# Optimization experiments

Measured on AMD Instinct MI355X. Metric: run time of the kernel, lower is better.

Reference implementation:

```python
import jax, jax.numpy as jnp
import numpy as np

E = 1024  # embed_dim
NH = 16   # num_heads
HH, WW = 128, 128


def setup_inputs() -> dict:
    key = jax.random.key(0)
    ks = jax.random.split(key, 9)
    s = 0.02
    x = jax.random.normal(ks[0], (1, HH, WW, E), dtype=jnp.float32)
    d = {"x": x}
    for i, name in enumerate(["q", "k", "v", "o"]):
        d[f"W{name}"] = jax.random.normal(ks[1 + 2 * i], (E, E), dtype=jnp.float32) * s
        d[f"b{name}"] = jax.random.normal(ks[2 + 2 * i], (E,), dtype=jnp.float32) * s
    return d


def reference(x, Wq, bq, Wk, bk, Wv, bv, Wo, bo):
    B, h, w, e = x.shape
    D = e // NH  # head dim
    # projections + ReLU feature map on q, k (torch Linear: x @ W.T + b)
    q = jnp.maximum(x @ Wq.T + bq, 0.0).reshape(B, h, w, NH, D)
    k = jnp.maximum(x @ Wk.T + bk, 0.0).reshape(B, h, w, NH, D)
    v = (x @ Wv.T + bv).reshape(B, h, w, NH, D)
    # width-axis linear retention: kv state per (row h, head n)
    kv_w = jnp.einsum('bhwnd,bhwne->bhnde', k, v)        # [B,h,NH,D,D]
    out = jnp.einsum('bhwnd,bhnde->bhwne', q, kv_w)      # [B,h,w,NH,D]
    # height-axis linear retention: kv state per (col w, head n)
    kv_h = jnp.einsum('bhwnd,bhwne->bwnde', k, v)        # [B,w,NH,D,D]
    out = jnp.einsum('bhwne,bwnef->bhwnf', out, kv_h)    # [B,h,w,NH,D]
    out = out.reshape(B, h, w, e) @ Wo.T + bo
    return out.reshape(B, h * w, e)
```

## Files before the change

### kernel.cpp

```cpp
#include <hip/hip_runtime.h>
#include <hip/hip_bf16.h>
#include <stdint.h>


typedef __attribute__((ext_vector_type(4))) float floatx4;
typedef __attribute__((ext_vector_type(8))) short shortx8;

static __device__ __forceinline__ unsigned short f2bf(float f) {
  unsigned int u = __float_as_uint(f);
  u += 0x7fffu + ((u >> 16) & 1u);
  return (unsigned short)(u >> 16);
}

static __device__ __forceinline__ void gload16(const void* g, void* l) {
  __builtin_amdgcn_global_load_lds(
      (const __attribute__((address_space(1))) void*)g,
      (__attribute__((address_space(3))) void*)l, 16, 0, 0);
}

__global__ __launch_bounds__(256) void cvt_all(
    const float* __restrict__ x, const float* __restrict__ Wq,
    const float* __restrict__ Wk, const float* __restrict__ Wv,
    const float* __restrict__ Wo, unsigned short* __restrict__ xb,
    unsigned short* __restrict__ wqkvb, unsigned short* __restrict__ wob) {
  const int b = blockIdx.x;
  const float* src;
  unsigned short* dst;
  int off;
  if (b < 16384) {
    src = x; dst = xb; off = b;
  } else if (b < 17408) {
    src = Wq; dst = wqkvb; off = b - 16384;
  } else if (b < 18432) {
    src = Wk; dst = wqkvb + 1048576; off = b - 17408;
  } else if (b < 19456) {
    src = Wv; dst = wqkvb + 2097152; off = b - 18432;
  } else {
    src = Wo; dst = wob; off = b - 19456;
  }
  const int i = (off * 256 + threadIdx.x) * 4;
  float4 f = *(const float4*)(src + i);
  ushort4 o;
  o.x = f2bf(f.x); o.y = f2bf(f.y); o.z = f2bf(f.z); o.w = f2bf(f.w);
  *(ushort4*)(dst + i) = o;
}

#define BARRIER()                           \
  do {                                      \
    asm volatile("" ::: "memory");          \
    __builtin_amdgcn_s_barrier();           \
    asm volatile("" ::: "memory");          \
  } while (0)
#define LGKM0 asm volatile("s_waitcnt lgkmcnt(0)" ::: "memory")
#define VMCNT(N) asm volatile("s_waitcnt vmcnt(" #N ")" ::: "memory")

template <int MODE>
__global__ __launch_bounds__(512, 2) void gemm256(
    const unsigned short* __restrict__ A,
    const unsigned short* __restrict__ BT,
    const float* __restrict__ b0, const float* __restrict__ b1,
    const float* __restrict__ b2,
    unsigned short* __restrict__ Oq, unsigned short* __restrict__ Ok,
    unsigned short* __restrict__ Ov, float* __restrict__ Of) {
  __shared__ __align__(16) unsigned short smem[65536];
  const int t = threadIdx.x;
  const int lane = t & 63, wid = t >> 6;
  const int wm = wid >> 2, wn = wid & 3;
  const int mrow = lane & 15, quad = lane >> 4;

  int bid = blockIdx.x, bm, bn;
  if (MODE == 0) {
    int s = (bid & 7) * 96 + (bid >> 3);
    bm = s / 12; bn = s - bm * 12;
  } else {
    int s = (bid & 7) * 32 + (bid >> 3);
    bm = s >> 2; bn = s & 3;
  }
  const int m0 = bm << 8;
  const int n0 = bn << 8;

  const int sw0 = ((quad ^ (mrow & 7)) << 3);
  const int sw1 = (((quad ^ 4) ^ (mrow & 7)) << 3);
  const int a_base = wm * 8192 + mrow * 64;
  const int b_base = 16384 + (wn >> 1) * 8192 + (((wn & 1) << 6) + mrow) * 64;
  const int s_dst0 = wid * 512 + lane * 8;
  const int srow = wid * 8 + (lane >> 3);
  const int csrc = ((lane & 7) ^ (lane >> 3)) << 3;
  const unsigned short* gAbase = A + (size_t)(m0 + srow) * 1024 + csrc;
  const unsigned short* gBbase = BT + (size_t)(n0 + srow) * 1024 + csrc;

#define STAGE_A(KT, H)                                              \
  do {                                                              \
    const unsigned short* _g = gAbase + ((H) << 17) + ((KT) << 6);  \
    const int _d = (((KT) & 1) << 15) + ((H) << 13) + s_dst0;       \
    gload16(_g, &smem[_d]);                                         \
    gload16(_g + 65536, &smem[_d + 4096]);                          \
  } while (0)
#define STAGE_B(KT, H)                                                     \
  do {                                                                     \
    const unsigned short* _g = gBbase + ((H) << 17) + ((KT) << 6);         \
    const int _d = (((KT) & 1) << 15) + 16384 + ((H) << 13) + s_dst0;      \
    gload16(_g, &smem[_d]);                                                \
    gload16(_g + 65536, &smem[_d + 4096]);                                 \
  } while (0)
#define LDA(MH)                                                  \
  do {                                                           \
    const int _ab = cb + a_base + ((MH) << 12);                  \
    _Pragma("unroll") for (int i = 0; i < 4; ++i) {              \
      aF[i][0] = *(const shortx8*)&smem[_ab + i * 1024 + sw0];   \
      aF[i][1] = *(const shortx8*)&smem[_ab + i * 1024 + sw1];   \
    }                                                            \
  } while (0)
#define LDB(NH)                                                      \
  do {                                                               \
    const int _bb = cb + b_base + ((NH) << 11);                      \
    _Pragma("unroll") for (int j = 0; j < 2; ++j) {                  \
      bF[NH][j][0] = *(const shortx8*)&smem[_bb + j * 1024 + sw0];   \
      bF[NH][j][1] = *(const shortx8*)&smem[_bb + j * 1024 + sw1];   \
    }                                                                \
  } while (0)
#define MFMAQ(MH, NH)                                                        \
  do {                                                                       \
    _Pragma("unroll") for (int ks = 0; ks < 2; ++ks)                         \
    _Pragma("unroll") for (int i = 0; i < 4; ++i)                            \
    _Pragma("unroll") for (int j = 0; j < 2; ++j)                            \
      acc[(MH) * 4 + i][(NH) * 2 + j] =                                      \
          __builtin_amdgcn_mfma_f32_16x16x32_bf16(                           \
              aF[i][ks], bF[NH][j][ks], acc[(MH) * 4 + i][(NH) * 2 + j], 0,  \
              0, 0);                                                         \
  } while (0)

  floatx4 acc[8][4] = {};
  shortx8 aF[4][2];
  shortx8 bF[2][2][2];

  STAGE_A(0, 0); STAGE_A(0, 1); STAGE_B(0, 0); STAGE_B(0, 1);
  __builtin_amdgcn_sched_barrier(0);
  VMCNT(0);
  __builtin_amdgcn_sched_barrier(0);
  STAGE_A(1, 0); STAGE_A(1, 1); STAGE_B(1, 0); STAGE_B(1, 1);
  BARRIER();

#pragma unroll 2
  for (int kt = 0; kt < 16; ++kt) {
    const int cb = (kt & 1) << 15;
    const bool pf = (kt < 14);
    LDA(0);
    LDB(0);
    BARRIER();
    LGKM0;
    __builtin_amdgcn_sched_barrier(0);
    __builtin_amdgcn_s_setprio(1);
    MFMAQ(0, 0);
    __builtin_amdgcn_s_setprio(0);
    BARRIER();
    LDB(1);
    BARRIER();
    LGKM0;
    __builtin_amdgcn_sched_barrier(0);
    __builtin_amdgcn_s_setprio(1);
    MFMAQ(0, 1);
    __builtin_amdgcn_s_setprio(0);
    BARRIER();
    LDA(1);
    if (pf) { STAGE_B(kt + 2, 0); STAGE_B(kt + 2, 1); }
    BARRIER();
    LGKM0;
    __builtin_amdgcn_sched_barrier(0);
    __builtin_amdgcn_s_setprio(1);
    MFMAQ(1, 1);
    __builtin_amdgcn_s_setprio(0);
    BARRIER();
    if (pf) { STAGE_A(kt + 2, 0); STAGE_A(kt + 2, 1); }
    __builtin_amdgcn_s_setprio(1);
    MFMAQ(1, 0);
    __builtin_amdgcn_s_setprio(0);
    if (pf) {
      VMCNT(8);
    } else {
      VMCNT(0);
    }
    BARRIER();
  }

  if (MODE == 0) {
    const int sel = n0 >> 10;
    const float* bb = (sel == 0) ? b0 : ((sel == 1) ? b1 : b2);
    unsigned short* O = (sel == 0) ? Oq : ((sel == 1) ? Ok : Ov);
    const int nb = n0 & 1023;
    float bias[4];
#pragma unroll
    for (int j = 0; j < 4; ++j) bias[j] = bb[nb + wn * 64 + j * 16 + mrow];
    unsigned short* we = &smem[wid * 8192];
#pragma unroll
    for (int mr = 0; mr < 8; ++mr)
#pragma unroll
      for (int j = 0; j < 4; ++j)
#pragma unroll
        for (int r = 0; r < 4; ++r) {
          const int row = mr * 16 + quad * 4 + r;
          const int col = j * 16 + mrow;
          float v = acc[mr][j][r] + bias[j];
          if (sel < 2) v = fmaxf(v, 0.0f);
          we[row * 64 + (((col >> 3) ^ (row & 7)) << 3) + (col & 7)] = f2bf(v);
        }
    __syncthreads();
#pragma unroll
    for (int it = 0; it < 16; ++it) {
      const int rr = it * 8 + (lane >> 3);
      const int cl = lane & 7;
      uint4 v = *(const uint4*)&we[rr * 64 + ((cl ^ (rr & 7)) << 3)];
      *(uint4*)&O[(size_t)(m0 + wm * 128 + rr) * 1024 + nb + wn * 64 + cl * 8] =
          v;
    }
  } else {
    float* wef = (float*)&smem[wid * 8192];
    float bias[4];
#pragma unroll
    for (int j = 0; j < 4; ++j) bias[j] = b0[n0 + wn * 64 + j * 16 + mrow];
#pragma unroll
    for (int h = 0; h < 2; ++h) {
#pragma unroll
      for (int i = 0; i < 4; ++i)
#pragma unroll
        for (int j = 0; j < 4; ++j)
#pragma unroll
          for (int r = 0; r < 4; ++r) {
            const int row = i * 16 + quad * 4 + r;
            const int col = j * 16 + mrow;
            wef[row * 64 + (((col >> 2) ^ (row & 7)) << 2) + (col & 3)] =
                acc[h * 4 + i][j][r] + bias[j];
          }
      __syncthreads();
#pragma unroll
      for (int it = 0; it < 16; ++it) {
        const int rr = it * 4 + (lane >> 4);
        const int cl = lane & 15;
        float4 v = *(const float4*)&wef[rr * 64 + ((cl ^ (rr & 7)) << 2)];
        *(float4*)&Of[(size_t)(m0 + wm * 128 + h * 64 + rr) * 1024 + n0 +
                      wn * 64 + cl * 4] = v;
      }
      __syncthreads();
    }
  }
#undef STAGE_A
#undef STAGE_B
#undef LDA
#undef LDB
#undef MFMAQ
}

__global__ __launch_bounds__(256) void retention_fused(
    const unsigned short* __restrict__ S, const unsigned short* __restrict__ Kb,
    const unsigned short* __restrict__ Vb, unsigned short* __restrict__ D,
    int axis) {
  const int outer = blockIdx.x;
  const int n = blockIdx.y;
  __shared__ unsigned short lS[128 * 72];
  __shared__ unsigned short lKT[64 * 136];
  __shared__ unsigned short lVT[64 * 136];
  unsigned short* lKV = lVT;
  const int t = threadIdx.x;
  const size_t base = (axis == 0) ? ((size_t)outer << 17) : ((size_t)outer << 10);
  const size_t istr = (axis == 0) ? (size_t)1024 : (size_t)131072;
  const size_t nof = (size_t)(n << 6);

#pragma unroll
  for (int it = 0; it < 4; ++it) {
    const int r = it * 32 + (t >> 3);
    const int c = (t & 7) * 8;
    uint4 v = *(const uint4*)&S[base + (size_t)r * istr + nof + c];
    *(uint4*)&lS[r * 72 + c] = v;
  }
#pragma unroll
  for (int it = 0; it < 4; ++it) {
    const int w = it * 32 + (t & 31);
    const int d0 = (t >> 5) * 8;
    const size_t g = base + (size_t)w * istr + nof + d0;
    uint4 k4 = *(const uint4*)&Kb[g];
    uint4 v4 = *(const uint4*)&Vb[g];
    const unsigned short* kp = (const unsigned short*)&k4;
    const unsigned short* vp = (const unsigned short*)&v4;
#pragma unroll
    for (int i = 0; i < 8; ++i) {
      lKT[(d0 + i) * 136 + w] = kp[i];
      lVT[(d0 + i) * 136 + w] = vp[i];
    }
  }
  __syncthreads();

  const int lane = t & 63;
  const int wv = t >> 6;
  const int mrow = lane & 15;
  const int quad = lane >> 4;

  floatx4 acc1[4] = {};
#pragma unroll
  for (int ks = 0; ks < 4; ++ks) {
    shortx8 a = *(const shortx8*)&lVT[(wv * 16 + mrow) * 136 + ks * 32 + quad * 8];
#pragma unroll
    for (int j = 0; j < 4; ++j) {
      shortx8 b = *(const shortx8*)&lKT[(j * 16 + mrow) * 136 + ks * 32 + quad * 8];
      acc1[j] = __builtin_amdgcn_mfma_f32_16x16x32_bf16(a, b, acc1[j], 0, 0, 0);
    }
  }
  __syncthreads();
#pragma unroll
  for (int j = 0; j < 4; ++j)
#pragma unroll
    for (int r = 0; r < 4; ++r)
      lKV[(wv * 16 + quad * 4 + r) * 72 + j * 16 + mrow] = f2bf(acc1[j][r]);
  __syncthreads();

  floatx4 acc2[2][4] = {};
#pragma unroll
  for (int ks = 0; ks < 2; ++ks) {
    shortx8 a2[2], b2[4];
#pragma unroll
    for (int i = 0; i < 2; ++i)
      a2[i] = *(const shortx8*)&lS[(wv * 32 + i * 16 + mrow) * 72 + ks * 32 + quad * 8];
#pragma unroll
    for (int j = 0; j < 4; ++j)
      b2[j] = *(const shortx8*)&lKV[(j * 16 + mrow) * 72 + ks * 32 + quad * 8];
#pragma unroll
    for (int i = 0; i < 2; ++i)
#pragma unroll
      for (int j = 0; j < 4; ++j)
        acc2[i][j] = __builtin_amdgcn_mfma_f32_16x16x32_bf16(a2[i], b2[j],
                                                             acc2[i][j], 0, 0, 0);
  }
  __syncthreads();
#pragma unroll
  for (int i = 0; i < 2; ++i)
#pragma unroll
    for (int j = 0; j < 4; ++j)
#pragma unroll
      for (int r = 0; r < 4; ++r) {
        const int row = wv * 32 + i * 16 + quad * 4 + r;
        const int col = j * 16 + mrow;
        lS[row * 72 + col] = f2bf(acc2[i][j][r]);
      }
  __syncthreads();
#pragma unroll
  for (int it = 0; it < 4; ++it) {
    const int row = it * 32 + (t >> 3);
    const int c = (t & 7) * 8;
    uint4 v = *(const uint4*)&lS[row * 72 + c];
    *(uint4*)&D[base + (size_t)row * istr + nof + c] = v;
  }
}

extern "C" void kernel_launch(void* const* d_in, const int* in_sizes, int n_in,
                              void* d_out, int out_size, void* d_ws, size_t ws_size,
                              hipStream_t stream) {
  const float* x  = (const float*)d_in[0];
  const float* Wq = (const float*)d_in[1];
  const float* bq = (const float*)d_in[2];
  const float* Wk = (const float*)d_in[3];
  const float* bk = (const float*)d_in[4];
  const float* Wv = (const float*)d_in[5];
  const float* bv = (const float*)d_in[6];
  const float* Wo = (const float*)d_in[7];
  const float* bo = (const float*)d_in[8];
  float* out = (float*)d_out;

  char* ws = (char*)d_ws;
  unsigned short* xb    = (unsigned short*)(ws + 0);
  unsigned short* wqkvb = (unsigned short*)(ws + 33554432);
  unsigned short* wob   = (unsigned short*)(ws + 39845888);
  unsigned short* qb    = (unsigned short*)(ws + 41943040);
  unsigned short* kb    = (unsigned short*)(ws + 75497472);
  unsigned short* vb    = (unsigned short*)(ws + 109051904);
  unsigned short* out1  = xb;
  unsigned short* out2  = qb;

  cvt_all<<<dim3(20480), dim3(256), 0, stream>>>(x, Wq, Wk, Wv, Wo, xb, wqkvb, wob);
  gemm256<0><<<dim3(768), dim3(512), 0, stream>>>(
      xb, wqkvb, bq, bk, bv, qb, kb, vb, (float*)nullptr);
  retention_fused<<<dim3(128, 16), dim3(256), 0, stream>>>(qb, kb, vb, out1, 0);
  retention_fused<<<dim3(128, 16), dim3(256), 0, stream>>>(out1, kb, vb, out2, 1);
  gemm256<1><<<dim3(256), dim3(512), 0, stream>>>(
      out2, wob, bo, nullptr, nullptr, nullptr, nullptr, nullptr, out);
}
```

Before: 330.7 us.

## Software-pipeline LDS fragment reads with MFMA using double-buffered register fragments

Restructures the GEMM main loop so LDS reads for the next quadrant (and the next k-tile's first fragments) are issued before the current MFMA block. Explicit lgkmcnt(0) waits and the extra barriers between loads and MFMAs are removed. Register fragments are double-buffered (aE/aO, bX/bY), and global prefetch is split across phases with finer vmcnt waits. The goal is to hide LDS latency behind matrix math. The cost is higher register pressure under launch bounds of 512 threads with 2 blocks, plus reliance on compiler-inserted waits for correctness.

```diff
diff --git a/kernel.cpp b/kernel.cpp
--- a/kernel.cpp
+++ b/kernel.cpp
@@ -51,7 +51,6 @@
     __builtin_amdgcn_s_barrier();           \
     asm volatile("" ::: "memory");          \
   } while (0)
-#define LGKM0 asm volatile("s_waitcnt lgkmcnt(0)" ::: "memory")
 #define VMCNT(N) asm volatile("s_waitcnt vmcnt(" #N ")" ::: "memory")
 
 template <int MODE>
@@ -103,36 +102,76 @@
     gload16(_g, &smem[_d]);                                                \
     gload16(_g + 65536, &smem[_d + 4096]);                                 \
   } while (0)
-#define LDA(MH)                                                  \
-  do {                                                           \
-    const int _ab = cb + a_base + ((MH) << 12);                  \
-    _Pragma("unroll") for (int i = 0; i < 4; ++i) {              \
-      aF[i][0] = *(const shortx8*)&smem[_ab + i * 1024 + sw0];   \
-      aF[i][1] = *(const shortx8*)&smem[_ab + i * 1024 + sw1];   \
-    }                                                            \
-  } while (0)
-#define LDB(NH)                                                      \
-  do {                                                               \
-    const int _bb = cb + b_base + ((NH) << 11);                      \
-    _Pragma("unroll") for (int j = 0; j < 2; ++j) {                  \
-      bF[NH][j][0] = *(const shortx8*)&smem[_bb + j * 1024 + sw0];   \
-      bF[NH][j][1] = *(const shortx8*)&smem[_bb + j * 1024 + sw1];   \
-    }                                                                \
-  } while (0)
-#define MFMAQ(MH, NH)                                                        \
-  do {                                                                       \
-    _Pragma("unroll") for (int ks = 0; ks < 2; ++ks)                         \
-    _Pragma("unroll") for (int i = 0; i < 4; ++i)                            \
-    _Pragma("unroll") for (int j = 0; j < 2; ++j)                            \
-      acc[(MH) * 4 + i][(NH) * 2 + j] =                                      \
-          __builtin_amdgcn_mfma_f32_16x16x32_bf16(                           \
-              aF[i][ks], bF[NH][j][ks], acc[(MH) * 4 + i][(NH) * 2 + j], 0,  \
-              0, 0);                                                         \
+#define RD_A(DST, CB, H)                                           \
+  do {                                                             \
+    const int _ab = (CB) + a_base + ((H) << 12);                   \
+    _Pragma("unroll") for (int i = 0; i < 4; ++i) {                \
+      DST[i][0] = *(const shortx8*)&smem[_ab + i * 1024 + sw0];    \
+      DST[i][1] = *(const shortx8*)&smem[_ab + i * 1024 + sw1];    \
+    }                                                              \
+  } while (0)
+#define RD_B(DST, CB, H)                                           \
+  do {                                                             \
+    const int _bb = (CB) + b_base + ((H) << 11);                   \
+    _Pragma("unroll") for (int j = 0; j < 2; ++j) {                \
+      DST[j][0] = *(const shortx8*)&smem[_bb + j * 1024 + sw0];    \
+      DST[j][1] = *(const shortx8*)&smem[_bb + j * 1024 + sw1];    \
+    }                                                              \
+  } while (0)
+#define MFMAQ(MH, NH, AS, BS)                                              \
+  do {                                                                     \
+    _Pragma("unroll") for (int ks = 0; ks < 2; ++ks)                       \
+    _Pragma("unroll") for (int i = 0; i < 4; ++i)                          \
+    _Pragma("unroll") for (int j = 0; j < 2; ++j)                          \
+      acc[(MH) * 4 + i][(NH) * 2 + j] =                                    \
+          __builtin_amdgcn_mfma_f32_16x16x32_bf16(                         \
+              AS[i][ks], BS[j][ks], acc[(MH) * 4 + i][(NH) * 2 + j], 0, 0, \
+              0);                                                          \
+  } while (0)
+
+#define KTILE(KT, BA, BB)                                          \
+  do {                                                             \
+    const int cb = ((KT) & 1) << 15;                               \
+    const int cbn = cb ^ 32768;                                    \
+    const bool pf = (KT) < 14;                                     \
+    const bool rd1 = (KT) < 15;                                    \
+                    \
+    RD_B(BB, cb, 1);                                               \
+    __builtin_amdgcn_s_setprio(1);                                 \
+    MFMAQ(0, 0, aE, BA);                                           \
+    __builtin_amdgcn_s_setprio(0);                                 \
+    BARRIER();                                                     \
+       \
+    RD_A(aO, cb, 1);                                               \
+    if (pf) {                                                      \
+      STAGE_A((KT) + 2, 0);                                        \
+      STAGE_B((KT) + 2, 0);                                        \
+      VMCNT(4);                                                    \
+    } else {                                                       \
+      VMCNT(0);                                                    \
+    }                                                              \
+    __builtin_amdgcn_s_setprio(1);                                 \
+    MFMAQ(0, 1, aE, BB);                                           \
+    __builtin_amdgcn_s_setprio(0);                                 \
+    BARRIER();                                                     \
+        \
+    if (rd1) RD_A(aE, cbn, 0);                                     \
+    if (pf) STAGE_B((KT) + 2, 1);                                  \
+    __builtin_amdgcn_s_setprio(1);                                 \
+    MFMAQ(1, 1, aO, BB);                                           \
+    __builtin_amdgcn_s_setprio(0);                                 \
+    BARRIER();                                                     \
+        \
+    if (rd1) RD_B(BB, cbn, 0);                                     \
+    if (pf) STAGE_A((KT) + 2, 1);                                  \
+    __builtin_amdgcn_s_setprio(1);                                 \
+    MFMAQ(1, 0, aO, BA);                                           \
+    __builtin_amdgcn_s_setprio(0);                                 \
+    BARRIER();                                                     \
   } while (0)
 
   floatx4 acc[8][4] = {};
-  shortx8 aF[4][2];
-  shortx8 bF[2][2][2];
+  shortx8 aE[4][2], aO[4][2], bX[2][2], bY[2][2];
 
   STAGE_A(0, 0); STAGE_A(0, 1); STAGE_B(0, 0); STAGE_B(0, 1);
   __builtin_amdgcn_sched_barrier(0);
@@ -140,47 +179,12 @@
   __builtin_amdgcn_sched_barrier(0);
   STAGE_A(1, 0); STAGE_A(1, 1); STAGE_B(1, 0); STAGE_B(1, 1);
   BARRIER();
-
-#pragma unroll 2
-  for (int kt = 0; kt < 16; ++kt) {
-    const int cb = (kt & 1) << 15;
-    const bool pf = (kt < 14);
-    LDA(0);
-    LDB(0);
-    BARRIER();
-    LGKM0;
-    __builtin_amdgcn_sched_barrier(0);
-    __builtin_amdgcn_s_setprio(1);
-    MFMAQ(0, 0);
-    __builtin_amdgcn_s_setprio(0);
-    BARRIER();
-    LDB(1);
-    BARRIER();
-    LGKM0;
-    __builtin_amdgcn_sched_barrier(0);
-    __builtin_amdgcn_s_setprio(1);
-    MFMAQ(0, 1);
-    __builtin_amdgcn_s_setprio(0);
-    BARRIER();
-    LDA(1);
-    if (pf) { STAGE_B(kt + 2, 0); STAGE_B(kt + 2, 1); }
-    BARRIER();
-    LGKM0;
-    __builtin_amdgcn_sched_barrier(0);
-    __builtin_amdgcn_s_setprio(1);
-    MFMAQ(1, 1);
-    __builtin_amdgcn_s_setprio(0);
-    BARRIER();
-    if (pf) { STAGE_A(kt + 2, 0); STAGE_A(kt + 2, 1); }
-    __builtin_amdgcn_s_setprio(1);
-    MFMAQ(1, 0);
-    __builtin_amdgcn_s_setprio(0);
-    if (pf) {
-      VMCNT(8);
-    } else {
-      VMCNT(0);
-    }
-    BARRIER();
+  RD_A(aE, 0, 0);
+  RD_B(bX, 0, 0);
+
+  for (int kt = 0; kt < 16; kt += 2) {
+    KTILE(kt, bX, bY);
+    KTILE(kt + 1, bY, bX);
   }
 
   if (MODE == 0) {
@@ -243,10 +247,11 @@
       __syncthreads();
     }
   }
+#undef KTILE
 #undef STAGE_A
 #undef STAGE_B
-#undef LDA
-#undef LDB
+#undef RD_A
+#undef RD_B
 #undef MFMAQ
 }
 
```

New measurement: 467.2 us. 1.41x slower.
